# Performance work log

Measured on AMD Instinct MI355X. Metric: run time of the kernel, lower is better.

Reference implementation:

```python
import jax, jax.numpy as jnp
import numpy as np

N_BASE = 10000.0  # frequency base from the module (self.N)


def setup_inputs() -> dict:
    key = jax.random.key(0)
    B, D = 16384, 2048
    # continuous timesteps in [0, 1000)
    t = jax.random.uniform(key, (B,), dtype=jnp.float32) * 1000.0
    return {"t": t, "D": D}


def reference(t, D):
    # i = 0 .. D/2 - 1 ; inv_freq = N ** (-2i/D)
    i = jnp.arange(D // 2, dtype=t.dtype)
    inv_freq = N_BASE ** (-2.0 * i / D)          # [D/2]
    ang = t[:, None] * inv_freq[None, :]          # [B, D/2]
    # interleave: even cols = sin, odd cols = cos
    emb = jnp.stack([jnp.sin(ang), jnp.cos(ang)], axis=-1)  # [B, D/2, 2]
    return emb.reshape(t.shape[0], D)             # [B, D]
```

## Files before the change

kernel.cpp:

```cpp
#include <hip/hip_runtime.h>


#define RPB 16

typedef float floatx4 __attribute__((ext_vector_type(4)));

__global__ __launch_bounds__(256) void sinpos_kernel(
    const float* __restrict__ t,
    floatx4* __restrict__ out,
    int q,
    float c)
{
    int j = blockIdx.x * blockDim.x + threadIdx.x;
    if (j >= q) return;
    int b0 = blockIdx.y * RPB;

    float i0 = (float)(2 * j);
    float f0 = __builtin_amdgcn_exp2f(c * i0);
    float f1 = __builtin_amdgcn_exp2f(c * (i0 + 1.0f));

    const float inv2pi = 0.15915494309189535f;
    float ts[RPB];
#pragma unroll
    for (int r = 0; r < RPB; ++r) ts[r] = t[b0 + r] * inv2pi;

    floatx4* p = out + (size_t)b0 * q + j;
#pragma unroll
    for (int r = 0; r < RPB; ++r) {
        float r0 = ts[r] * f0; r0 -= __builtin_floorf(r0);
        float r1 = ts[r] * f1; r1 -= __builtin_floorf(r1);
        floatx4 v;
        v.x = __builtin_amdgcn_sinf(r0);
        v.y = __builtin_amdgcn_cosf(r0);
        v.z = __builtin_amdgcn_sinf(r1);
        v.w = __builtin_amdgcn_cosf(r1);
        __builtin_nontemporal_store(v, p);
        p += q;
    }
}

extern "C" void kernel_launch(void* const* d_in, const int* in_sizes, int n_in,
                              void* d_out, int out_size, void* d_ws, size_t ws_size,
                              hipStream_t stream) {
    const float* t = (const float*)d_in[0];
    float* out = (float*)d_out;

    int B = in_sizes[0];
    int D = out_size / B;
    int q = D / 4;

    float c = (float)(-2.0 * 13.287712379549449 / (double)D);

    dim3 block(256);
    dim3 grid((q + 255) / 256, B / RPB);
    sinpos_kernel<<<grid, block, 0, stream>>>(t, (floatx4*)out, q, c);
}
```

Baseline: 141.1 us.

## Map each wavefront to full rows and drop nontemporal stores

```diff
diff --git a/kernel.cpp b/kernel.cpp
--- a/kernel.cpp
+++ b/kernel.cpp
@@ -1,41 +1,46 @@
 #include <hip/hip_runtime.h>
 
 
-#define RPB 16
-
-typedef float floatx4 __attribute__((ext_vector_type(4)));
+#define RPW 8
+#define NW  8
 
 __global__ __launch_bounds__(256) void sinpos_kernel(
     const float* __restrict__ t,
-    floatx4* __restrict__ out,
+    float4* __restrict__ out,
     int q,
     float c)
 {
-    int j = blockIdx.x * blockDim.x + threadIdx.x;
-    if (j >= q) return;
-    int b0 = blockIdx.y * RPB;
+    int lane = threadIdx.x & 63;
+    int wid  = blockIdx.x * 4 + (threadIdx.x >> 6);
+    int b0   = wid * RPW;
 
-    float i0 = (float)(2 * j);
-    float f0 = __builtin_amdgcn_exp2f(c * i0);
-    float f1 = __builtin_amdgcn_exp2f(c * (i0 + 1.0f));
+    float f0[NW], f1[NW];
+#pragma unroll
+    for (int w = 0; w < NW; ++w) {
+        float i0 = (float)(2 * (w * 64 + lane));
+        f0[w] = __builtin_amdgcn_exp2f(c * i0);
+        f1[w] = __builtin_amdgcn_exp2f(c * (i0 + 1.0f));
+    }
 
     const float inv2pi = 0.15915494309189535f;
-    float ts[RPB];
+    float ts[RPW];
 #pragma unroll
-    for (int r = 0; r < RPB; ++r) ts[r] = t[b0 + r] * inv2pi;
+    for (int r = 0; r < RPW; ++r) ts[r] = t[b0 + r] * inv2pi;
 
-    floatx4* p = out + (size_t)b0 * q + j;
+    float4* p = out + (size_t)b0 * q + lane;
 #pragma unroll
-    for (int r = 0; r < RPB; ++r) {
-        float r0 = ts[r] * f0; r0 -= __builtin_floorf(r0);
-        float r1 = ts[r] * f1; r1 -= __builtin_floorf(r1);
-        floatx4 v;
-        v.x = __builtin_amdgcn_sinf(r0);
-        v.y = __builtin_amdgcn_cosf(r0);
-        v.z = __builtin_amdgcn_sinf(r1);
-        v.w = __builtin_amdgcn_cosf(r1);
-        __builtin_nontemporal_store(v, p);
-        p += q;
+    for (int r = 0; r < RPW; ++r) {
+#pragma unroll
+        for (int w = 0; w < NW; ++w) {
+            float r0 = ts[r] * f0[w]; r0 -= __builtin_floorf(r0);
+            float r1 = ts[r] * f1[w]; r1 -= __builtin_floorf(r1);
+            float4 v;
+            v.x = __builtin_amdgcn_sinf(r0);
+            v.y = __builtin_amdgcn_cosf(r0);
+            v.z = __builtin_amdgcn_sinf(r1);
+            v.w = __builtin_amdgcn_cosf(r1);
+            p[(r * NW + w) * 64] = v;
+        }
     }
 }
 
@@ -52,6 +57,6 @@
     float c = (float)(-2.0 * 13.287712379549449 / (double)D);
 
     dim3 block(256);
-    dim3 grid((q + 255) / 256, B / RPB);
-    sinpos_kernel<<<grid, block, 0, stream>>>(t, (floatx4*)out, q, c);
+    dim3 grid(B / (RPW * 4));
+    sinpos_kernel<<<grid, block, 0, stream>>>(t, (float4*)out, q, c);
 }
```

Result: faster. 133.8 us (median of 2 runs) (-5.2%).
